# Performance work log

Measured on AMD Instinct MI355X. Metric: run time of the kernel, lower is better.

The kernel has to match this reference:

```python
import jax, jax.numpy as jnp
import numpy as np

B, C_IN, C_INT, H, W = 8, 512, 256, 128, 128


def setup_inputs() -> dict:
    key = jax.random.key(0)
    k1, k2, k3, k4, k5, k6 = jax.random.split(key, 6)
    energy = jax.random.normal(k1, (B, C_INT, C_INT), dtype=jnp.float32)
    x = jax.random.normal(k2, (B, C_IN, H, W), dtype=jnp.float32)
    # 1x1 conv params (kernel_size=1 -> plain channel-mixing matrices)
    sv = 1.0 / np.sqrt(C_IN)
    sr = 1.0 / np.sqrt(C_INT)
    w_value = jax.random.uniform(k3, (C_INT, C_IN), jnp.float32, -sv, sv)
    b_value = jax.random.uniform(k4, (C_INT,), jnp.float32, -sv, sv)
    w_re = jax.random.uniform(k5, (C_IN, C_INT), jnp.float32, -sr, sr)
    b_re = jax.random.uniform(k6, (C_IN,), jnp.float32, -sr, sr)
    # gamma initialized to zeros in the torch module; use small nonzero so
    # the attention branch contributes to the output for kernel testing.
    gamma = jnp.full((1,), 0.1, dtype=jnp.float32)
    return {"energy": energy, "x": x, "w_value": w_value, "b_value": b_value,
            "w_re": w_re, "b_re": b_re, "gamma": gamma}


def reference(energy, x, w_value, b_value, w_re, b_re, gamma):
    b, _, h, w = x.shape
    # value = value_conv(x): 1x1 conv == channel GEMM  [B,Cin,H,W] -> [B,Cint,H,W]
    value = jnp.einsum('oc,bchw->bohw', w_value, x) + b_value[None, :, None, None]
    value = value.reshape(b, C_INT, h * w)                 # [B, Cint, HW]
    attention = jax.nn.softmax(energy, axis=-1)            # [B, Cint, Cint]
    # dropout is identity in eval mode (reference baseline is deterministic)
    out = jnp.einsum('bij,bjn->bin', attention, value)     # [B, Cint, HW]
    out = out.reshape(b, C_INT, h, w)
    # value_reconv: 1x1 conv back to in_channel
    out = jnp.einsum('oc,bchw->bohw', w_re, out) + b_re[None, :, None, None]
    out = gamma * out + x
    out = out + x
    return out
```

## Files before the change

kernel.cpp:

```cpp
#include <hip/hip_runtime.h>

typedef unsigned short ushort_t;
typedef __attribute__((ext_vector_type(8))) __bf16 bf16x8;
typedef __attribute__((ext_vector_type(8))) ushort_t u16x8;
typedef __attribute__((ext_vector_type(4))) float f32x4;

__device__ __forceinline__ ushort_t f2bf(float f) {
  union { float f; unsigned int u; } v; v.f = f;
  unsigned int u = v.u;
  u += 0x7fffu + ((u >> 16) & 1u);
  return (ushort_t)(u >> 16);
}

__global__ __launch_bounds__(64) void softmax_k(
    const float* __restrict__ energy, const float* __restrict__ bval,
    float* __restrict__ Asm, float* __restrict__ u)
{
  const int row = blockIdx.x;
  const int l = threadIdx.x;
  const float* e = energy + (size_t)row * 256;
  float v0 = e[l], v1 = e[l + 64], v2 = e[l + 128], v3 = e[l + 192];
  float mx = fmaxf(fmaxf(v0, v1), fmaxf(v2, v3));
  #pragma unroll
  for (int o = 32; o > 0; o >>= 1) mx = fmaxf(mx, __shfl_xor(mx, o));
  v0 = __expf(v0 - mx); v1 = __expf(v1 - mx);
  v2 = __expf(v2 - mx); v3 = __expf(v3 - mx);
  float s = v0 + v1 + v2 + v3;
  #pragma unroll
  for (int o = 32; o > 0; o >>= 1) s += __shfl_xor(s, o);
  const float inv = 1.0f / s;
  v0 *= inv; v1 *= inv; v2 *= inv; v3 *= inv;
  float* Ao = Asm + (size_t)row * 256;
  Ao[l] = v0; Ao[l + 64] = v1; Ao[l + 128] = v2; Ao[l + 192] = v3;
  float ub = v0 * bval[l] + v1 * bval[l + 64] + v2 * bval[l + 128] + v3 * bval[l + 192];
  #pragma unroll
  for (int o = 32; o > 0; o >>= 1) ub += __shfl_xor(ub, o);
  if (l == 0) u[row] = ub;
}

__global__ __launch_bounds__(256) void gemm_f32(
    const float* __restrict__ A, int lda, int sA,
    const float* __restrict__ B, int ldb, int sB,
    float* __restrict__ C, int ldc, int sC, int K)
{
  const int bz = blockIdx.z;
  A += (size_t)bz * sA; B += (size_t)bz * sB; C += (size_t)bz * sC;
  const int m0 = blockIdx.y * 64, n0 = blockIdx.x * 64;
  __shared__ float As[64][17];
  __shared__ float Bs[16][65];
  const int t = threadIdx.x, tx = t & 15, ty = t >> 4;
  float acc[4][4] = {};
  for (int k0 = 0; k0 < K; k0 += 16) {
    {
      const int r = t >> 2, kc = (t & 3) * 4;
      float4 av = *(const float4*)(A + (size_t)(m0 + r) * lda + k0 + kc);
      As[r][kc] = av.x; As[r][kc + 1] = av.y; As[r][kc + 2] = av.z; As[r][kc + 3] = av.w;
      const int rr = t >> 4, cc = (t & 15) * 4;
      float4 bv = *(const float4*)(B + (size_t)(k0 + rr) * ldb + n0 + cc);
      Bs[rr][cc] = bv.x; Bs[rr][cc + 1] = bv.y; Bs[rr][cc + 2] = bv.z; Bs[rr][cc + 3] = bv.w;
    }
    __syncthreads();
    #pragma unroll
    for (int kk = 0; kk < 16; ++kk) {
      float a[4], bb[4];
      #pragma unroll
      for (int i = 0; i < 4; ++i) a[i] = As[ty * 4 + i][kk];
      #pragma unroll
      for (int j = 0; j < 4; ++j) bb[j] = Bs[kk][tx * 4 + j];
      #pragma unroll
      for (int i = 0; i < 4; ++i)
        #pragma unroll
        for (int j = 0; j < 4; ++j) acc[i][j] += a[i] * bb[j];
    }
    __syncthreads();
  }
  #pragma unroll
  for (int i = 0; i < 4; ++i)
    #pragma unroll
    for (int j = 0; j < 4; ++j)
      C[(size_t)(m0 + ty * 4 + i) * ldc + n0 + tx * 4 + j] = acc[i][j];
}

__global__ __launch_bounds__(256) void bias_k(
    const float* __restrict__ wre, const float* __restrict__ u,
    const float* __restrict__ bre, const float* __restrict__ gp,
    float* __restrict__ c)
{
  const int idx = blockIdx.x * 256 + threadIdx.x;
  const int b = idx >> 9, o = idx & 511;
  const float* wrow = wre + (size_t)o * 256;
  const float* uu = u + b * 256;
  float s = 0.f;
  for (int j = 0; j < 256; ++j) s += wrow[j] * uu[j];
  c[idx] = gp[0] * (s + bre[o]);
}

__global__ __launch_bounds__(256) void pswz_k(
    const float* __restrict__ P, const float* __restrict__ gp,
    ushort_t* __restrict__ Ps)
{
  const int d = blockIdx.x * 256 + threadIdx.x;
  const int j = d & 7, lane = (d >> 3) & 63, mt = (d >> 9) & 31;
  const int kt = (d >> 14) & 15, b = d >> 18;
  const int kg = lane >> 4, mr = lane & 15;
  const int m = mt * 16 + mr, k = kt * 32 + kg * 8 + j;
  Ps[d] = f2bf(gp[0] * P[((size_t)b * 512 + m) * 512 + k]);
}

__global__ __launch_bounds__(256) void main_k(
    const ushort_t* __restrict__ Ps, const float* __restrict__ x,
    const float* __restrict__ cvec, float* __restrict__ out)
{
  __shared__ __align__(16) ushort_t Blds[2][8192];
  __shared__ float clds[128];

  const int bid = blockIdx.x;
  const int b = bid & 7;
  const int yb = (bid >> 3) & 3;
  const int n0 = (bid >> 5) * 128;
  const int m0 = yb * 128;

  const int t = threadIdx.x, lane = t & 63;
  const int w = t >> 6, wr = w >> 1, wc = w & 1;

  if (t < 128) clds[t] = cvec[b * 512 + m0 + t];

  const float* xb = x + (size_t)b * (512 * 16384);
  const int c4 = t & 31;
  const int r0 = (t >> 5) * 8;
  const int xcol = n0 + 4 * c4;

  f32x4 acc[4][4];
  #pragma unroll
  for (int i = 0; i < 4; ++i)
    #pragma unroll
    for (int j = 0; j < 4; ++j) acc[i][j] = (f32x4){0.f, 0.f, 0.f, 0.f};

  float4 stg[8];

  auto loadTile = [&](int kt) {
    #pragma unroll
    for (int i = 0; i < 8; ++i)
      stg[i] = *(const float4*)(xb + (size_t)(kt * 64 + r0 + i) * 16384 + xcol);
  };
  auto writeTile = [&](int bufI) {
    char* base = (char*)&Blds[bufI][0];
    #pragma unroll
    for (int cc = 0; cc < 4; ++cc) {
      const int col = 4 * c4 + cc;
      u16x8 tmp;
      #pragma unroll
      for (int i = 0; i < 8; ++i) {
        const float* fv = (const float*)&stg[i];
        tmp[i] = f2bf(fv[cc]);
      }
      const int swz = ((col >> 2) ^ col) & 7;
      const int off = col * 128 + ((r0 * 2) ^ (swz << 4));
      *(u16x8*)(base + off) = tmp;
    }
  };

  loadTile(0);
  writeTile(0);
  __syncthreads();

  const int mtb = yb * 8 + wr * 4;

  #pragma unroll
  for (int kt = 0; kt < 8; ++kt) {
    const int cur = kt & 1;
    if (kt < 7) loadTile(kt + 1);

    bf16x8 af[2][4];
    #pragma unroll
    for (int kk = 0; kk < 2; ++kk)
      #pragma unroll
      for (int i = 0; i < 4; ++i) {
        const size_t off = ((size_t)((b * 16 + (kt * 2 + kk)) * 32 + (mtb + i))) * 512
                         + (size_t)lane * 8;
        af[kk][i] = *(const bf16x8*)(Ps + off);
      }

    const char* base = (const char*)&Blds[cur][0];
    #pragma unroll
    for (int kk = 0; kk < 2; ++kk) {
      #pragma unroll
      for (int j = 0; j < 4; ++j) {
        const int col = wc * 64 + j * 16 + (lane & 15);
        const int kb = kk * 64 + (lane >> 4) * 16;
        const int swz = ((col >> 2) ^ col) & 7;
        const bf16x8 bf = *(const bf16x8*)(base + col * 128 + (kb ^ (swz << 4)));
        #pragma unroll
        for (int i = 0; i < 4; ++i)
          acc[i][j] = __builtin_amdgcn_mfma_f32_16x16x32_bf16(af[kk][i], bf, acc[i][j], 0, 0, 0);
      }
    }

    if (kt < 7) writeTile(cur ^ 1);
    __syncthreads();
  }

  float* ob = out + (size_t)b * (512 * 16384);
  #pragma unroll
  for (int i = 0; i < 4; ++i) {
    #pragma unroll
    for (int r = 0; r < 4; ++r) {
      const int lm = wr * 64 + i * 16 + (lane >> 4) * 4 + r;
      const size_t gm = (size_t)(m0 + lm);
      const float cb = clds[lm];
      #pragma unroll
      for (int j = 0; j < 4; ++j) {
        const int gn = n0 + wc * 64 + j * 16 + (lane & 15);
        const size_t off = gm * 16384 + gn;
        ob[off] = fmaf(2.0f, xb[off], acc[i][j][r] + cb);
      }
    }
  }
}

extern "C" void kernel_launch(void* const* d_in, const int* in_sizes, int n_in,
                              void* d_out, int out_size, void* d_ws, size_t ws_size,
                              hipStream_t stream) {
  const float* energy  = (const float*)d_in[0];
  const float* x       = (const float*)d_in[1];
  const float* w_value = (const float*)d_in[2];
  const float* b_value = (const float*)d_in[3];
  const float* w_re    = (const float*)d_in[4];
  const float* b_re    = (const float*)d_in[5];
  const float* gamma   = (const float*)d_in[6];
  float* out = (float*)d_out;

  char* ws = (char*)d_ws;
  float*    Asm = (float*)(ws);
  float*    u   = (float*)(ws + 2097152);
  float*    T   = (float*)(ws + 2105344);
  float*    P   = (float*)(ws + 6299648);
  float*    c   = (float*)(ws + 14688256);
  ushort_t* Ps  = (ushort_t*)(ws + 14704640);

  softmax_k<<<2048, 64, 0, stream>>>(energy, b_value, Asm, u);
  gemm_f32<<<dim3(4, 8, 8), 256, 0, stream>>>(w_re, 256, 0,
                                              Asm, 256, 256 * 256,
                                              T, 256, 512 * 256, 256);
  gemm_f32<<<dim3(8, 8, 8), 256, 0, stream>>>(T, 256, 512 * 256,
                                              w_value, 512, 0,
                                              P, 512, 512 * 512, 256);
  bias_k<<<16, 256, 0, stream>>>(w_re, u, b_re, gamma, c);
  pswz_k<<<8192, 256, 0, stream>>>(P, gamma, Ps);
  main_k<<<4096, 256, 0, stream>>>(Ps, x, c, out);
}
```

Measured before the change: 632.7 us.

## Deepen prefetch pipeline in main kernel and vectorize small fp32 GEMM

The main MFMA kernel now prefetches x tiles two iterations ahead and double-buffers the A-fragment register loads, with sched barriers to order LDS writes, global loads and MFMAs. The fp32-to-bf16 packing uses the hardware v_cvt_pk_bf16_f32 instruction instead of manual rounding, and the bias is read directly from global memory instead of staged through LDS. The small fp32 GEMMs get a transposed A tile with float4 LDS reads and vector stores. Together these aim to hide global-load latency in the memory-bound main kernel and cut ALU and LDS overhead, at the cost of more registers and possible occupancy loss.

```diff
diff --git a/kernel.cpp b/kernel.cpp
--- a/kernel.cpp
+++ b/kernel.cpp
@@ -4,12 +4,19 @@
 typedef __attribute__((ext_vector_type(8))) __bf16 bf16x8;
 typedef __attribute__((ext_vector_type(8))) ushort_t u16x8;
 typedef __attribute__((ext_vector_type(4))) float f32x4;
+typedef __attribute__((ext_vector_type(4))) unsigned int u32x4;
 
 __device__ __forceinline__ ushort_t f2bf(float f) {
   union { float f; unsigned int u; } v; v.f = f;
   unsigned int u = v.u;
   u += 0x7fffu + ((u >> 16) & 1u);
   return (ushort_t)(u >> 16);
+}
+
+__device__ __forceinline__ unsigned cvt_pk_bf16(float lo, float hi) {
+  unsigned r;
+  asm("v_cvt_pk_bf16_f32 %0, %1, %2" : "=v"(r) : "v"(lo), "v"(hi));
+  return r;
 }
 
 __global__ __launch_bounds__(64) void softmax_k(
@@ -38,7 +45,7 @@
   if (l == 0) u[row] = ub;
 }
 
-__global__ __launch_bounds__(256) void gemm_f32(
+__global__ __launch_bounds__(256) void gemm2_k(
     const float* __restrict__ A, int lda, int sA,
     const float* __restrict__ B, int ldb, int sB,
     float* __restrict__ C, int ldc, int sC, int K)
@@ -46,39 +53,37 @@
   const int bz = blockIdx.z;
   A += (size_t)bz * sA; B += (size_t)bz * sB; C += (size_t)bz * sC;
   const int m0 = blockIdx.y * 64, n0 = blockIdx.x * 64;
-  __shared__ float As[64][17];
-  __shared__ float Bs[16][65];
+  __shared__ float AsT[16][68];
+  __shared__ float Bs[16][68];
   const int t = threadIdx.x, tx = t & 15, ty = t >> 4;
+  const int ar = t >> 2, ak = (t & 3) * 4;
+  const int br = t >> 4, bc = (t & 15) * 4;
   float acc[4][4] = {};
   for (int k0 = 0; k0 < K; k0 += 16) {
-    {
-      const int r = t >> 2, kc = (t & 3) * 4;
-      float4 av = *(const float4*)(A + (size_t)(m0 + r) * lda + k0 + kc);
-      As[r][kc] = av.x; As[r][kc + 1] = av.y; As[r][kc + 2] = av.z; As[r][kc + 3] = av.w;
-      const int rr = t >> 4, cc = (t & 15) * 4;
-      float4 bv = *(const float4*)(B + (size_t)(k0 + rr) * ldb + n0 + cc);
-      Bs[rr][cc] = bv.x; Bs[rr][cc + 1] = bv.y; Bs[rr][cc + 2] = bv.z; Bs[rr][cc + 3] = bv.w;
-    }
+    float4 av = *(const float4*)(A + (size_t)(m0 + ar) * lda + k0 + ak);
+    float4 bv = *(const float4*)(B + (size_t)(k0 + br) * ldb + n0 + bc);
     __syncthreads();
+    AsT[ak][ar] = av.x; AsT[ak + 1][ar] = av.y;
+    AsT[ak + 2][ar] = av.z; AsT[ak + 3][ar] = av.w;
+    *(float4*)&Bs[br][bc] = bv;
+    __syncthreads();
     #pragma unroll
     for (int kk = 0; kk < 16; ++kk) {
-      float a[4], bb[4];
-      #pragma unroll
-      for (int i = 0; i < 4; ++i) a[i] = As[ty * 4 + i][kk];
-      #pragma unroll
-      for (int j = 0; j < 4; ++j) bb[j] = Bs[kk][tx * 4 + j];
+      float4 a4 = *(const float4*)&AsT[kk][ty * 4];
+      float4 b4 = *(const float4*)&Bs[kk][tx * 4];
+      const float aa[4] = {a4.x, a4.y, a4.z, a4.w};
+      const float bb[4] = {b4.x, b4.y, b4.z, b4.w};
       #pragma unroll
       for (int i = 0; i < 4; ++i)
         #pragma unroll
-        for (int j = 0; j < 4; ++j) acc[i][j] += a[i] * bb[j];
-    }
-    __syncthreads();
-  }
-  #pragma unroll
-  for (int i = 0; i < 4; ++i)
-    #pragma unroll
-    for (int j = 0; j < 4; ++j)
-      C[(size_t)(m0 + ty * 4 + i) * ldc + n0 + tx * 4 + j] = acc[i][j];
+        for (int j = 0; j < 4; ++j) acc[i][j] = fmaf(aa[i], bb[j], acc[i][j]);
+    }
+  }
+  #pragma unroll
+  for (int i = 0; i < 4; ++i) {
+    float4 cv = {acc[i][0], acc[i][1], acc[i][2], acc[i][3]};
+    *(float4*)(C + (size_t)(m0 + ty * 4 + i) * ldc + n0 + tx * 4) = cv;
+  }
 }
 
 __global__ __launch_bounds__(256) void bias_k(
@@ -112,7 +117,6 @@
     const float* __restrict__ cvec, float* __restrict__ out)
 {
   __shared__ __align__(16) ushort_t Blds[2][8192];
-  __shared__ float clds[128];
 
   const int bid = blockIdx.x;
   const int b = bid & 7;
@@ -123,12 +127,11 @@
   const int t = threadIdx.x, lane = t & 63;
   const int w = t >> 6, wr = w >> 1, wc = w & 1;
 
-  if (t < 128) clds[t] = cvec[b * 512 + m0 + t];
-
   const float* xb = x + (size_t)b * (512 * 16384);
   const int c4 = t & 31;
   const int r0 = (t >> 5) * 8;
   const int xcol = n0 + 4 * c4;
+  const int mtb = yb * 8 + wr * 4;
 
   f32x4 acc[4][4];
   #pragma unroll
@@ -137,51 +140,58 @@
     for (int j = 0; j < 4; ++j) acc[i][j] = (f32x4){0.f, 0.f, 0.f, 0.f};
 
   float4 stg[8];
+  bf16x8 afA[8], afB[8];
 
   auto loadTile = [&](int kt) {
     #pragma unroll
     for (int i = 0; i < 8; ++i)
       stg[i] = *(const float4*)(xb + (size_t)(kt * 64 + r0 + i) * 16384 + xcol);
   };
+  auto loadA = [&](int kt, bf16x8* dst) {
+    #pragma unroll
+    for (int kk = 0; kk < 2; ++kk)
+      #pragma unroll
+      for (int i = 0; i < 4; ++i)
+        dst[kk * 4 + i] = *(const bf16x8*)(
+            Ps + ((size_t)((b * 16 + (kt * 2 + kk)) * 32 + (mtb + i))) * 512
+               + (size_t)lane * 8);
+  };
   auto writeTile = [&](int bufI) {
     char* base = (char*)&Blds[bufI][0];
     #pragma unroll
     for (int cc = 0; cc < 4; ++cc) {
       const int col = 4 * c4 + cc;
-      u16x8 tmp;
-      #pragma unroll
-      for (int i = 0; i < 8; ++i) {
-        const float* fv = (const float*)&stg[i];
-        tmp[i] = f2bf(fv[cc]);
+      u32x4 wv;
+      #pragma unroll
+      for (int p = 0; p < 4; ++p) {
+        const float* f0 = (const float*)&stg[2 * p];
+        const float* f1 = (const float*)&stg[2 * p + 1];
+        wv[p] = cvt_pk_bf16(f0[cc], f1[cc]);
       }
       const int swz = ((col >> 2) ^ col) & 7;
       const int off = col * 128 + ((r0 * 2) ^ (swz << 4));
-      *(u16x8*)(base + off) = tmp;
+      *(u32x4*)(base + off) = wv;
     }
   };
 
+  loadA(0, afA);
+  loadA(1, afB);
   loadTile(0);
   writeTile(0);
+  loadTile(1);
   __syncthreads();
 
-  const int mtb = yb * 8 + wr * 4;
-
   #pragma unroll
   for (int kt = 0; kt < 8; ++kt) {
-    const int cur = kt & 1;
-    if (kt < 7) loadTile(kt + 1);
-
-    bf16x8 af[2][4];
-    #pragma unroll
-    for (int kk = 0; kk < 2; ++kk)
-      #pragma unroll
-      for (int i = 0; i < 4; ++i) {
-        const size_t off = ((size_t)((b * 16 + (kt * 2 + kk)) * 32 + (mtb + i))) * 512
-                         + (size_t)lane * 8;
-        af[kk][i] = *(const bf16x8*)(Ps + off);
-      }
-
-    const char* base = (const char*)&Blds[cur][0];
+    bf16x8* cur = (kt & 1) ? afB : afA;
+
+    if (kt < 7) writeTile((kt + 1) & 1);
+    __builtin_amdgcn_sched_barrier(0);
+
+    if (kt < 6) loadTile(kt + 2);
+    __builtin_amdgcn_sched_barrier(0);
+
+    const char* base = (const char*)&Blds[kt & 1][0];
     #pragma unroll
     for (int kk = 0; kk < 2; ++kk) {
       #pragma unroll
@@ -192,22 +202,23 @@
         const bf16x8 bf = *(const bf16x8*)(base + col * 128 + (kb ^ (swz << 4)));
         #pragma unroll
         for (int i = 0; i < 4; ++i)
-          acc[i][j] = __builtin_amdgcn_mfma_f32_16x16x32_bf16(af[kk][i], bf, acc[i][j], 0, 0, 0);
+          acc[i][j] = __builtin_amdgcn_mfma_f32_16x16x32_bf16(cur[kk * 4 + i], bf, acc[i][j], 0, 0, 0);
       }
     }
 
-    if (kt < 7) writeTile(cur ^ 1);
+    if (kt < 6) loadA(kt + 2, cur);
     __syncthreads();
   }
 
   float* ob = out + (size_t)b * (512 * 16384);
+  const float* cb_base = cvec + b * 512 + m0;
   #pragma unroll
   for (int i = 0; i < 4; ++i) {
     #pragma unroll
     for (int r = 0; r < 4; ++r) {
       const int lm = wr * 64 + i * 16 + (lane >> 4) * 4 + r;
       const size_t gm = (size_t)(m0 + lm);
-      const float cb = clds[lm];
+      const float cb = cb_base[lm];
       #pragma unroll
       for (int j = 0; j < 4; ++j) {
         const int gn = n0 + wc * 64 + j * 16 + (lane & 15);
@@ -239,12 +250,12 @@
   ushort_t* Ps  = (ushort_t*)(ws + 14704640);
 
   softmax_k<<<2048, 64, 0, stream>>>(energy, b_value, Asm, u);
-  gemm_f32<<<dim3(4, 8, 8), 256, 0, stream>>>(w_re, 256, 0,
-                                              Asm, 256, 256 * 256,
-                                              T, 256, 512 * 256, 256);
-  gemm_f32<<<dim3(8, 8, 8), 256, 0, stream>>>(T, 256, 512 * 256,
-                                              w_value, 512, 0,
-                                              P, 512, 512 * 512, 256);
+  gemm2_k<<<dim3(4, 8, 8), 256, 0, stream>>>(w_re, 256, 0,
+                                             Asm, 256, 256 * 256,
+                                             T, 256, 512 * 256, 256);
+  gemm2_k<<<dim3(8, 8, 8), 256, 0, stream>>>(T, 256, 512 * 256,
+                                             w_value, 512, 0,
+                                             P, 512, 512 * 512, 256);
   bias_k<<<16, 256, 0, stream>>>(w_re, u, b_re, gamma, c);
   pswz_k<<<8192, 256, 0, stream>>>(P, gamma, Ps);
   main_k<<<4096, 256, 0, stream>>>(Ps, x, c, out);
```

Result: slower. 673.2 us (+6.4%).
